# Optimization experiments

Hardware: AMD Instinct MI355X
Metric: run time of the kernel (lower is better)

## Reference

```python
import jax, jax.numpy as jnp
import numpy as np

EPS = 1e-6


def _rmsnorm(x, w, eps=EPS):
    # x: (..., d); normalize over last dim
    ms = jnp.mean(jnp.square(x), axis=-1, keepdims=True)
    return x * jax.lax.rsqrt(ms + eps) * w


def setup_inputs() -> dict:
    key = jax.random.key(0)
    ks = jax.random.split(key, 5)
    B, S, D = 2, 2048, 2048
    n_heads, n_kv = 16, 4
    d_head = D // n_heads  # 128
    sd = 1.0 / np.sqrt(D)
    return {
        "x": jax.random.normal(ks[0], (B, S, D), dtype=jnp.float32),
        "wq": jax.random.normal(ks[1], (D, n_heads * d_head), dtype=jnp.float32) * sd,
        "wk": jax.random.normal(ks[2], (D, n_kv * d_head), dtype=jnp.float32) * sd,
        "wv": jax.random.normal(ks[3], (D, n_kv * d_head), dtype=jnp.float32) * sd,
        "wo": jax.random.normal(ks[4], (D, D), dtype=jnp.float32) * sd,
        "q_norm_w": jnp.ones((d_head,), dtype=jnp.float32),
        "k_norm_w": jnp.ones((d_head,), dtype=jnp.float32),
    }


def reference(x, wq, wk, wv, wo, q_norm_w, k_norm_w):
    B, S, D = x.shape
    n_heads, n_kv = 16, 4
    groups = n_heads // n_kv
    d_head = D // n_heads

    # QKV projections (bias=False)
    q = (x @ wq).reshape(B, S, n_kv, groups, d_head)  # q heads grouped by kv head
    k = (x @ wk).reshape(B, S, n_kv, d_head)
    v = (x @ wv).reshape(B, S, n_kv, d_head)

    # qk RMSNorm over d_head
    q = _rmsnorm(q, q_norm_w)
    k = _rmsnorm(k, k_norm_w)

    # GQA attention without materializing expanded K/V:
    # scores: (B, n_kv, groups, S_q, S_k)
    scale = 1.0 / jnp.sqrt(jnp.asarray(d_head, dtype=x.dtype))
    scores = jnp.einsum('bskgd,btkd->bkgst', q, k) * scale
    causal = jnp.tril(jnp.ones((S, S), dtype=bool))
    scores = jnp.where(causal, scores, jnp.asarray(-jnp.inf, dtype=scores.dtype))
    attn = jax.nn.softmax(scores, axis=-1)
    out = jnp.einsum('bkgst,btkd->bskgd', attn, v)  # (B, S, n_kv, groups, d_head)
    out = out.reshape(B, S, D)
    return out @ wo
```

## Files before the change

### kernel.cpp

```cpp
#include <hip/hip_runtime.h>
#include <hip/hip_bf16.h>
#include <stdint.h>

typedef unsigned short u16;
typedef __attribute__((ext_vector_type(8))) short short8;
typedef __attribute__((ext_vector_type(4))) float f32x4;
typedef __attribute__((ext_vector_type(16))) float f32x16;

__device__ __forceinline__ u16 f2bf(float f){
  union { __hip_bfloat16 h; u16 u; } v; v.h = __float2bfloat16(f); return v.u;
}
__device__ __forceinline__ float bf2f(u16 h){
  union { uint32_t u; float f; } v; v.u = ((uint32_t)h) << 16;
  return v.f;
}
__device__ __forceinline__ f32x4 mfma16(short8 a, short8 b, f32x4 c){
  return __builtin_amdgcn_mfma_f32_16x16x32_bf16(a, b, c, 0, 0, 0);
}
__device__ __forceinline__ f32x16 mfma32(short8 a, short8 b, f32x16 c){
  return __builtin_amdgcn_mfma_f32_32x32x16_bf16(a, b, c, 0, 0, 0);
}
__device__ __forceinline__ void gl_lds16(const u16* g, u16* l){
  __builtin_amdgcn_global_load_lds((const __attribute__((address_space(1))) void*)g,
                                   (__attribute__((address_space(3))) void*)l, 16, 0, 0);
}
template<int N> __device__ __forceinline__ void waitvm(){
  if constexpr (N==0) asm volatile("s_waitcnt vmcnt(0)" ::: "memory");
  else if constexpr (N==4) asm volatile("s_waitcnt vmcnt(4)" ::: "memory");
  else if constexpr (N==8) asm volatile("s_waitcnt vmcnt(8)" ::: "memory");
  else static_assert(N==0 || N==4 || N==8, "unsupported vmcnt");
}
__device__ __forceinline__ void phase_sep(){
  __builtin_amdgcn_sched_barrier(0);
  __builtin_amdgcn_s_barrier();
  __builtin_amdgcn_sched_barrier(0);
}
__device__ __forceinline__ uint32_t cvtpk(float lo, float hi){
  uint32_t r;
  asm("v_cvt_pk_bf16_f32 %0, %1, %2" : "=v"(r) : "v"(lo), "v"(hi));
  return r;
}

__global__ __launch_bounds__(256) void cvt_x(const float* __restrict__ s,
                                             u16* __restrict__ d, int n4){
  const int i = blockIdx.x*256 + threadIdx.x;
  if (i >= n4) return;
  const float4 v = ((const float4*)s)[i];
  ushort4 pk;
  pk.x = f2bf(v.x); pk.y = f2bf(v.y); pk.z = f2bf(v.z); pk.w = f2bf(v.w);
  ((ushort4*)d)[i] = pk;
}

__global__ __launch_bounds__(256) void transpose_cvt(const float* __restrict__ src,
    u16* __restrict__ dst, int R, int C)
{
  __shared__ float tile[32][33];
  const int tx = threadIdx.x, ty = threadIdx.y;
  const int c0 = blockIdx.x << 5, r0 = blockIdx.y << 5;
  #pragma unroll
  for (int i=0;i<4;i++)
    tile[ty + (i<<3)][tx] = src[(size_t)(r0 + ty + (i<<3))*C + c0 + tx];
  __syncthreads();
  #pragma unroll
  for (int i=0;i<4;i++)
    dst[(size_t)(c0 + ty + (i<<3))*R + r0 + tx] = f2bf(tile[tx][ty + (i<<3)]);
}

__global__ __launch_bounds__(256) void v_transpose(const u16* __restrict__ qkv,
    u16* __restrict__ vT)
{
  __shared__ u16 tile[32][33];
  const int tx = threadIdx.x, ty = threadIdx.y;
  const int s0 = blockIdx.x << 5, d0 = blockIdx.y << 5;
  const int bk = blockIdx.z; const int b = bk >> 2, kv = bk & 3;
  const u16* src = qkv + (size_t)b*2048*3072 + 2560 + kv*128;
  #pragma unroll
  for (int i=0;i<4;i++)
    tile[ty + (i<<3)][tx] = src[(size_t)(s0 + ty + (i<<3))*3072 + d0 + tx];
  __syncthreads();
  u16* dst = vT + (size_t)((b<<2)+kv)*128*2048;
  #pragma unroll
  for (int i=0;i<4;i++)
    dst[(size_t)(d0 + ty + (i<<3))*2048 + s0 + tx] = tile[tx][ty + (i<<3)];
}

__global__ __launch_bounds__(256) void rmsnorm_qk(u16* __restrict__ qkv,
    const float* __restrict__ qw, const float* __restrict__ kw)
{
  const int lane = threadIdx.x & 63;
  const int rid = blockIdx.x*4 + (threadIdx.x >> 6);
  const int row = rid / 20;
  const int slot = rid % 20;
  u16* p = qkv + (size_t)row*3072 + slot*128 + (lane<<1);
  const u16 r0 = p[0], r1 = p[1];
  const float a = bf2f(r0), c = bf2f(r1);
  float ss = a*a + c*c;
  #pragma unroll
  for (int off=1; off<64; off<<=1) ss += __shfl_xor(ss, off);
  float sc = rsqrtf(ss*(1.0f/128.0f) + 1e-6f);
  if (slot < 16) sc *= 0.1275187952317199f;
  const float* wp = (slot < 16) ? qw : kw;
  const float w0 = wp[lane<<1], w1 = wp[(lane<<1)+1];
  p[0] = f2bf(a*sc*w0);
  p[1] = f2bf(c*sc*w1);
}

template<int CBF16>
__global__ __launch_bounds__(512, 2) void gemm8(const u16* __restrict__ A,
    const u16* __restrict__ BT, void* __restrict__ Cp,
    int M, int N, int K, int ldc)
{
  __shared__ u16 lds[65536];
  const int tid = threadIdx.x;
  const int w = tid >> 6, lane = tid & 63;
  const int l15 = lane & 15, lg = lane >> 4;
  const int wm = w >> 2, wn = w & 3;
  const int nbx = N >> 8;
  const int nwg = gridDim.x;
  int bid = blockIdx.x;
  bid = (bid & 7) * (nwg >> 3) + (bid >> 3);
  const int m0 = (bid / nbx) << 8;
  const int n0 = (bid % nbx) << 8;

  const u16* gA0 = A  + (size_t)m0*K;
  const u16* gA1 = gA0 + (size_t)128*K;
  const u16* gB0 = BT + (size_t)n0*K;
  const u16* gB1 = gB0 + (size_t)128*K;

  auto slot = [&](int d, int s)->u16*{ return lds + (((d<<2)+s)<<13); };

  auto stage_half = [&](const u16* gbase, int kt, u16* sbase){
    #pragma unroll
    for (int i=0;i<2;i++){
      const int p = (i<<9) + tid;
      const int row = p>>3, sg = (p&7) ^ (row&7);
      gl_lds16(gbase + (size_t)row*K + (kt<<6) + (sg<<3), sbase + (p<<3));
    }
  };
  auto frag_at = [&](const u16* buf, int lrow, int kk)->short8{
    const int s = ((kk<<2)+lg) ^ (lrow&7);
    return *(const short8*)(buf + (((lrow<<3)+s)<<3));
  };

  short8 af[4][2], bfe[2][2], bfo[2][2];
  f32x4 acc[8][4];
  #pragma unroll
  for (int m=0;m<8;m++)
    #pragma unroll
    for (int n=0;n<4;n++) acc[m][n] = (f32x4){0.f,0.f,0.f,0.f};

  const int bh = 2 + (wn>>1);
  const int brow0 = ((wn&1)<<6) + l15;

  auto rd_a = [&](const u16* buf, int mq){
    #pragma unroll
    for (int m=0;m<4;m++)
      #pragma unroll
      for (int kk=0;kk<2;kk++)
        af[m][kk] = frag_at(buf, (mq<<6) + (m<<4) + l15, kk);
  };
  auto rd_b = [&](const u16* buf, int nq, short8 (*dst)[2]){
    #pragma unroll
    for (int n=0;n<2;n++)
      #pragma unroll
      for (int kk=0;kk<2;kk++)
        dst[n][kk] = frag_at(buf, brow0 + (nq<<5) + (n<<4), kk);
  };
  auto do_mfma = [&](int mb, int nb, short8 (*bf)[2]){
    __builtin_amdgcn_s_setprio(1);
    #pragma unroll
    for (int m=0;m<4;m++)
      #pragma unroll
      for (int n=0;n<2;n++)
        #pragma unroll
        for (int kk=0;kk<2;kk++)
          acc[mb+m][nb+n] = mfma16(af[m][kk], bf[n][kk], acc[mb+m][nb+n]);
    __builtin_amdgcn_s_setprio(0);
  };

  stage_half(gA0, 0, slot(0,0)); stage_half(gA1, 0, slot(0,1));
  stage_half(gB0, 0, slot(0,2)); stage_half(gB1, 0, slot(0,3));
  stage_half(gA0, 1, slot(1,0)); stage_half(gA1, 1, slot(1,1));
  waitvm<4>();
  phase_sep();

  const int niter = K >> 7;
  for (int i=0; i<niter; ++i){
    const bool full = (i+1 < niter);
    const int t1 = 2*i+1;
    rd_a(slot(0,wm), 0); rd_b(slot(0,bh), 0, bfe);
    stage_half(gB0, t1, slot(1,2)); stage_half(gB1, t1, slot(1,3));
    phase_sep();
    do_mfma(0, 0, bfe);
    phase_sep();
    rd_b(slot(0,bh), 1, bfo);
    phase_sep();
    do_mfma(0, 2, bfo);
    phase_sep();
    rd_a(slot(0,wm), 1);
    phase_sep();
    do_mfma(4, 2, bfo);
    phase_sep();
    rd_b(slot(0,bh), 0, bfe);
    if (full){ stage_half(gA0, t1+1, slot(0,0)); stage_half(gA1, t1+1, slot(0,1)); }
    phase_sep();
    do_mfma(4, 0, bfe);
    if (full) waitvm<4>(); else waitvm<0>();
    phase_sep();
    rd_a(slot(1,wm), 0); rd_b(slot(1,bh), 0, bfe);
    if (full){ stage_half(gB0, t1+1, slot(0,2)); stage_half(gB1, t1+1, slot(0,3)); }
    phase_sep();
    do_mfma(0, 0, bfe);
    phase_sep();
    rd_b(slot(1,bh), 1, bfo);
    phase_sep();
    do_mfma(0, 2, bfo);
    phase_sep();
    rd_a(slot(1,wm), 1);
    phase_sep();
    do_mfma(4, 2, bfo);
    phase_sep();
    rd_b(slot(1,bh), 0, bfe);
    if (full){ stage_half(gA0, t1+2, slot(1,0)); stage_half(gA1, t1+2, slot(1,1)); }
    phase_sep();
    do_mfma(4, 0, bfe);
    if (full) waitvm<4>();
    phase_sep();
  }

  #pragma unroll
  for (int m=0;m<8;m++){
    #pragma unroll
    for (int n=0;n<4;n++){
      const int col = n0 + (wn<<6) + (n<<4) + l15;
      #pragma unroll
      for (int r=0;r<4;r++){
        const int row = m0 + (wm<<7) + (m<<4) + (lg<<2) + r;
        if (CBF16) ((u16*)Cp)[(size_t)row*ldc + col] = f2bf(acc[m][n][r]);
        else       ((float*)Cp)[(size_t)row*ldc + col] = acc[m][n][r];
      }
    }
  }
}

__global__ __launch_bounds__(256, 2) void attn_kernel(const u16* __restrict__ qkv,
    const u16* __restrict__ vT, u16* __restrict__ aout)
{
  __shared__ u16 Klds[2][8192];
  __shared__ u16 Vlds[8192];
  const int tid = threadIdx.x;
  const int w = tid >> 6, lane = tid & 63;
  const int l31 = lane & 31, hi = lane >> 5;
  const int bx = blockIdx.x, h = blockIdx.y, b = blockIdx.z;
  const int qI = b ? bx : (15 - bx);
  const int kvh = h >> 2;
  const int qb = qI*128 + (w<<5);
  const int nt = 2*qI + 2;

  const u16* qkvb = qkv + (size_t)b*2048*3072;
  short8 qf[8];
  {
    const u16* qp = qkvb + (size_t)(qb + l31)*3072 + h*128 + hi*8;
    #pragma unroll
    for (int kk=0;kk<8;kk++) qf[kk] = *(const short8*)(qp + kk*16);
  }
  f32x16 oacc[4];
  #pragma unroll
  for (int d=0;d<4;d++)
    #pragma unroll
    for (int r=0;r<16;r++) oacc[d][r] = 0.f;
  float m_run = -__builtin_inff(), lsum = 0.f;

  const u16* kb_ = qkvb + 2048 + kvh*128;
  const u16* vb_ = vT + (size_t)((b<<2)+kvh)*128*2048;

  auto stageK = [&](int t, int buf){
    #pragma unroll
    for (int i=0;i<4;i++){
      const int u = (i<<8) + tid;
      const int row = u>>4, d0 = (u&15) ^ (row&15);
      gl_lds16(kb_ + (size_t)((t<<6)+row)*3072 + (d0<<3), &Klds[buf][u<<3]);
    }
  };
  auto stageV = [&](int t){
    #pragma unroll
    for (int i=0;i<4;i++){
      const int u = (i<<8) + tid;
      const int rp = u>>4, z = (u&15) ^ (rp&15);
      const int d = (rp<<1) + (z>>3), k8 = z&7;
      gl_lds16(vb_ + (size_t)d*2048 + (t<<6) + (k8<<3), &Vlds[u<<3]);
    }
  };

  stageK(0, 0);
  int kbuf = 0;
  for (int t=0; t<nt; ++t){
    const bool pre = (t+1 < nt);
    stageV(t);
    if (pre) stageK(t+1, kbuf^1);
    if (pre) waitvm<8>(); else waitvm<4>();
    phase_sep();
    const int t0 = t<<6;
    const bool act = (t0 <= qb + 31);
    uint32_t paw[4][4];
    if (act){
      f32x16 s0, s1;
      #pragma unroll
      for (int r=0;r<16;r++){ s0[r] = 0.f; s1[r] = 0.f; }
      #pragma unroll
      for (int kk=0;kk<8;kk++){
        const int d0 = (kk<<1) + hi;
        const short8 k0 = *(const short8*)&Klds[kbuf][((l31<<4) + (d0 ^ (l31&15)))<<3];
        s0 = mfma32(k0, qf[kk], s0);
        const int r1 = 32 + l31;
        const short8 k1 = *(const short8*)&Klds[kbuf][((r1<<4) + (d0 ^ (r1&15)))<<3];
        s1 = mfma32(k1, qf[kk], s1);
      }
      if (t0 + 63 > qb){
        const int qrel = qb + l31 - t0;
        #pragma unroll
        for (int r=0;r<16;r++){
          const int kloc = (r&3) + ((r>>2)<<3) + (hi<<2);
          if (kloc      > qrel) s0[r] = -__builtin_inff();
          if (kloc + 32 > qrel) s1[r] = -__builtin_inff();
        }
      }
      float t8[8];
      #pragma unroll
      for (int i=0;i<8;i++) t8[i] = fmaxf(fmaxf(s0[i], s0[i+8]), fmaxf(s1[i], s1[i+8]));
      #pragma unroll
      for (int i=0;i<4;i++) t8[i] = fmaxf(t8[i], t8[i+4]);
      float mx = fmaxf(fmaxf(t8[0],t8[1]), fmaxf(t8[2],t8[3]));
      mx = fmaxf(mx, __shfl_xor(mx, 32));
      const bool noskip = !__all(mx - m_run <= 8.0f);
      const float mnew = noskip ? fmaxf(m_run, mx) : m_run;
      float rs = 0.f;
      #pragma unroll
      for (int i=0;i<16;i++){
        s0[i] = __builtin_amdgcn_exp2f(s0[i] - mnew);
        s1[i] = __builtin_amdgcn_exp2f(s1[i] - mnew);
        rs += s0[i] + s1[i];
      }
      rs += __shfl_xor(rs, 32);
      if (noskip){
        const float corr = __builtin_amdgcn_exp2f(m_run - mnew);
        m_run = mnew;
        lsum = lsum*corr + rs;
        #pragma unroll
        for (int r=0;r<16;r++){
          const float cr = __shfl(corr, (r&3) + ((r>>2)<<3) + (hi<<2));
          #pragma unroll
          for (int db=0;db<4;db++) oacc[db][r] *= cr;
        }
      } else {
        lsum += rs;
      }
      #pragma unroll
      for (int kk=0;kk<4;kk++){
        const int base = (kk&1)<<3;
        float v0,v1,v2,v3,v4,v5,v6,v7;
        if (kk<2){ v0=s0[base+0]; v1=s0[base+1]; v2=s0[base+2]; v3=s0[base+3];
                   v4=s0[base+4]; v5=s0[base+5]; v6=s0[base+6]; v7=s0[base+7]; }
        else     { v0=s1[base+0]; v1=s1[base+1]; v2=s1[base+2]; v3=s1[base+3];
                   v4=s1[base+4]; v5=s1[base+5]; v6=s1[base+6]; v7=s1[base+7]; }
        uint32_t a0 = cvtpk(v0, v1), a1 = cvtpk(v2, v3);
        uint32_t b0 = cvtpk(v4, v5), b1 = cvtpk(v6, v7);
        asm volatile("v_permlane32_swap_b32 %0, %1" : "+v"(a0), "+v"(b0));
        asm volatile("v_permlane32_swap_b32 %0, %1" : "+v"(a1), "+v"(b1));
        paw[kk][0] = a0; paw[kk][1] = a1; paw[kk][2] = b0; paw[kk][3] = b1;
      }
    }
    if (pre) waitvm<4>(); else waitvm<0>();
    phase_sep();
    if (act){
      #pragma unroll
      for (int kk=0;kk<4;kk++){
        union { uint32_t w[4]; short8 v; } pu;
        pu.w[0]=paw[kk][0]; pu.w[1]=paw[kk][1]; pu.w[2]=paw[kk][2]; pu.w[3]=paw[kk][3];
        const short8 pa = pu.v;
        #pragma unroll
        for (int db=0;db<4;db++){
          const int d = (db<<5) + l31, rp = d>>1;
          const int sl = (((d&1)<<3) | ((kk<<1)+hi)) ^ (rp&15);
          const short8 vv = *(const short8*)&Vlds[((rp<<4)+sl)<<3];
          oacc[db] = mfma32(pa, vv, oacc[db]);
        }
      }
    }
    phase_sep();
    kbuf ^= 1;
  }

  const float inv = 1.0f / lsum;
  #pragma unroll
  for (int r=0;r<16;r++){
    const int qr = (r&3) + ((r>>2)<<3) + (hi<<2);
    const float ivr = __shfl(inv, qr);
    u16* op = aout + (size_t)(b*2048 + qb + qr)*2048 + h*128 + l31;
    #pragma unroll
    for (int db=0;db<4;db++)
      op[db<<5] = f2bf(oacc[db][r] * ivr);
  }
}

extern "C" void kernel_launch(void* const* d_in, const int* in_sizes, int n_in,
                              void* d_out, int out_size, void* d_ws, size_t ws_size,
                              hipStream_t stream) {
  const float* x  = (const float*)d_in[0];
  const float* wq = (const float*)d_in[1];
  const float* wk = (const float*)d_in[2];
  const float* wv = (const float*)d_in[3];
  const float* wo = (const float*)d_in[4];
  const float* qw = (const float*)d_in[5];
  const float* kw = (const float*)d_in[6];
  char* ws = (char*)d_ws;
  u16* xbf   = (u16*)(ws);
  u16* wqkvT = (u16*)(ws + 16777216);
  u16* woT   = (u16*)(ws + 29360128);
  u16* qkv   = (u16*)(ws + 37748736);
  u16* vT    = (u16*)(ws + 62914560);
  float* out = (float*)d_out;

  dim3 tb(32,8);
  cvt_x<<<8192, 256, 0, stream>>>(x, xbf, 2097152);
  transpose_cvt<<<dim3(64,64), tb, 0, stream>>>(wq, wqkvT,             2048, 2048);
  transpose_cvt<<<dim3(16,64), tb, 0, stream>>>(wk, wqkvT + 2048*2048, 2048, 512);
  transpose_cvt<<<dim3(16,64), tb, 0, stream>>>(wv, wqkvT + 2560*2048, 2048, 512);
  transpose_cvt<<<dim3(64,64), tb, 0, stream>>>(wo, woT,               2048, 2048);
  gemm8<1><<<192, 512, 0, stream>>>(xbf, wqkvT, qkv, 4096, 3072, 2048, 3072);
  rmsnorm_qk<<<20480, 256, 0, stream>>>(qkv, qw, kw);
  v_transpose<<<dim3(64,4,8), tb, 0, stream>>>(qkv, vT);
  attn_kernel<<<dim3(16,16,2), 256, 0, stream>>>(qkv, vT, xbf);
  gemm8<0><<<128, 512, 0, stream>>>(xbf, woT, out, 4096, 2048, 2048, 2048);
}
```

Before: 214.0 us.

## Pair high and low query tiles per block and double-buffer K/V staging

Each wave now handles 16 query rows from a high tile and 16 from a mirrored low tile, so every block runs the same number of key tiles (32 - p) and causal work stays balanced. The per-tile activity skip is removed, and masking now runs on every tile. V gets its own double buffer alongside K, and tiles are prefetched two steps ahead with a single wait per iteration, which removes the mid-iteration V wait. The cost is double the LDS for V, which may lower occupancy, plus masking and exp work on tiles where the low rows are fully masked.

New measurement: 229.8 us. +7.4%, slower.

```diff
diff --git a/kernel.cpp b/kernel.cpp
--- a/kernel.cpp
+++ b/kernel.cpp
@@ -247,20 +247,21 @@
     const u16* __restrict__ vT, u16* __restrict__ aout)
 {
   __shared__ u16 Klds[2][8192];
-  __shared__ u16 Vlds[8192];
+  __shared__ u16 Vlds[2][8192];
   const int tid = threadIdx.x;
   const int w = tid >> 6, lane = tid & 63;
   const int l31 = lane & 31, hi = lane >> 5;
   const int bx = blockIdx.x, h = blockIdx.y, b = blockIdx.z;
-  const int qI = b ? bx : (15 - bx);
+  const int p_eff = b ? (15 - bx) : bx;
   const int kvh = h >> 2;
-  const int qb = qI*128 + (w<<5);
-  const int nt = 2*qI + 2;
+  const int hq0 = (31 - p_eff) << 6, lq0 = p_eff << 6;
+  const int nt = 32 - p_eff;
+  const int qrow = (l31 < 16) ? (hq0 + (w<<4) + l31) : (lq0 + (w<<4) + l31 - 16);
 
   const u16* qkvb = qkv + (size_t)b*2048*3072;
   short8 qf[8];
   {
-    const u16* qp = qkvb + (size_t)(qb + l31)*3072 + h*128 + hi*8;
+    const u16* qp = qkvb + (size_t)qrow*3072 + h*128 + hi*8;
     #pragma unroll
     for (int kk=0;kk<8;kk++) qf[kk] = *(const short8*)(qp + kk*16);
   }
@@ -274,129 +275,119 @@
   const u16* kb_ = qkvb + 2048 + kvh*128;
   const u16* vb_ = vT + (size_t)((b<<2)+kvh)*128*2048;
 
-  auto stageK = [&](int t, int buf){
+  auto stageKV = [&](int t, int buf){
     #pragma unroll
     for (int i=0;i<4;i++){
       const int u = (i<<8) + tid;
       const int row = u>>4, d0 = (u&15) ^ (row&15);
       gl_lds16(kb_ + (size_t)((t<<6)+row)*3072 + (d0<<3), &Klds[buf][u<<3]);
     }
-  };
-  auto stageV = [&](int t){
     #pragma unroll
     for (int i=0;i<4;i++){
       const int u = (i<<8) + tid;
       const int rp = u>>4, z = (u&15) ^ (rp&15);
       const int d = (rp<<1) + (z>>3), k8 = z&7;
-      gl_lds16(vb_ + (size_t)d*2048 + (t<<6) + (k8<<3), &Vlds[u<<3]);
-    }
-  };
-
-  stageK(0, 0);
-  int kbuf = 0;
+      gl_lds16(vb_ + (size_t)d*2048 + (t<<6) + (k8<<3), &Vlds[buf][u<<3]);
+    }
+  };
+
+  stageKV(0, 0);
+  if (nt > 1) stageKV(1, 1);
   for (int t=0; t<nt; ++t){
-    const bool pre = (t+1 < nt);
-    stageV(t);
-    if (pre) stageK(t+1, kbuf^1);
-    if (pre) waitvm<8>(); else waitvm<4>();
+    const int kbuf = t & 1;
+    if (t+1 < nt) waitvm<8>(); else waitvm<0>();
     phase_sep();
     const int t0 = t<<6;
-    const bool act = (t0 <= qb + 31);
+    f32x16 s0, s1;
+    #pragma unroll
+    for (int r=0;r<16;r++){ s0[r] = 0.f; s1[r] = 0.f; }
+    #pragma unroll
+    for (int kk=0;kk<8;kk++){
+      const int d0 = (kk<<1) + hi;
+      const short8 k0 = *(const short8*)&Klds[kbuf][((l31<<4) + (d0 ^ (l31&15)))<<3];
+      s0 = mfma32(k0, qf[kk], s0);
+      const int r1 = 32 + l31;
+      const short8 k1 = *(const short8*)&Klds[kbuf][((r1<<4) + (d0 ^ (r1&15)))<<3];
+      s1 = mfma32(k1, qf[kk], s1);
+    }
+    {
+      const int qrel = qrow - t0;
+      #pragma unroll
+      for (int r=0;r<16;r++){
+        const int kloc = (r&3) + ((r>>2)<<3) + (hi<<2);
+        if (kloc      > qrel) s0[r] = -__builtin_inff();
+        if (kloc + 32 > qrel) s1[r] = -__builtin_inff();
+      }
+    }
+    float t8[8];
+    #pragma unroll
+    for (int i=0;i<8;i++) t8[i] = fmaxf(fmaxf(s0[i], s0[i+8]), fmaxf(s1[i], s1[i+8]));
+    #pragma unroll
+    for (int i=0;i<4;i++) t8[i] = fmaxf(t8[i], t8[i+4]);
+    float mx = fmaxf(fmaxf(t8[0],t8[1]), fmaxf(t8[2],t8[3]));
+    mx = fmaxf(mx, __shfl_xor(mx, 32));
+    const bool noskip = !__all(mx - m_run <= 8.0f);
+    const float mnew = noskip ? fmaxf(m_run, mx) : m_run;
+    float rs = 0.f;
+    #pragma unroll
+    for (int i=0;i<16;i++){
+      s0[i] = __builtin_amdgcn_exp2f(s0[i] - mnew);
+      s1[i] = __builtin_amdgcn_exp2f(s1[i] - mnew);
+      rs += s0[i] + s1[i];
+    }
+    rs += __shfl_xor(rs, 32);
+    if (noskip){
+      const float corr = __builtin_amdgcn_exp2f(m_run - mnew);
+      m_run = mnew;
+      lsum = lsum*corr + rs;
+      #pragma unroll
+      for (int r=0;r<16;r++){
+        const float cr = __shfl(corr, (r&3) + ((r>>2)<<3) + (hi<<2));
+        #pragma unroll
+        for (int db=0;db<4;db++) oacc[db][r] *= cr;
+      }
+    } else {
+      lsum += rs;
+    }
     uint32_t paw[4][4];
-    if (act){
-      f32x16 s0, s1;
-      #pragma unroll
-      for (int r=0;r<16;r++){ s0[r] = 0.f; s1[r] = 0.f; }
-      #pragma unroll
-      for (int kk=0;kk<8;kk++){
-        const int d0 = (kk<<1) + hi;
-        const short8 k0 = *(const short8*)&Klds[kbuf][((l31<<4) + (d0 ^ (l31&15)))<<3];
-        s0 = mfma32(k0, qf[kk], s0);
-        const int r1 = 32 + l31;
-        const short8 k1 = *(const short8*)&Klds[kbuf][((r1<<4) + (d0 ^ (r1&15)))<<3];
-        s1 = mfma32(k1, qf[kk], s1);
+    #pragma unroll
+    for (int kk=0;kk<4;kk++){
+      const int base = (kk&1)<<3;
+      float v0,v1,v2,v3,v4,v5,v6,v7;
+      if (kk<2){ v0=s0[base+0]; v1=s0[base+1]; v2=s0[base+2]; v3=s0[base+3];
+                 v4=s0[base+4]; v5=s0[base+5]; v6=s0[base+6]; v7=s0[base+7]; }
+      else     { v0=s1[base+0]; v1=s1[base+1]; v2=s1[base+2]; v3=s1[base+3];
+                 v4=s1[base+4]; v5=s1[base+5]; v6=s1[base+6]; v7=s1[base+7]; }
+      uint32_t a0 = cvtpk(v0, v1), a1 = cvtpk(v2, v3);
+      uint32_t b0 = cvtpk(v4, v5), b1 = cvtpk(v6, v7);
+      asm volatile("v_permlane32_swap_b32 %0, %1" : "+v"(a0), "+v"(b0));
+      asm volatile("v_permlane32_swap_b32 %0, %1" : "+v"(a1), "+v"(b1));
+      paw[kk][0] = a0; paw[kk][1] = a1; paw[kk][2] = b0; paw[kk][3] = b1;
+    }
+    #pragma unroll
+    for (int kk=0;kk<4;kk++){
+      union { uint32_t w[4]; short8 v; } pu;
+      pu.w[0]=paw[kk][0]; pu.w[1]=paw[kk][1]; pu.w[2]=paw[kk][2]; pu.w[3]=paw[kk][3];
+      const short8 pa = pu.v;
+      #pragma unroll
+      for (int db=0;db<4;db++){
+        const int d = (db<<5) + l31, rp = d>>1;
+        const int sl = (((d&1)<<3) | ((kk<<1)+hi)) ^ (rp&15);
+        const short8 vv = *(const short8*)&Vlds[kbuf][((rp<<4)+sl)<<3];
+        oacc[db] = mfma32(pa, vv, oacc[db]);
       }
-      if (t0 + 63 > qb){
-        const int qrel = qb + l31 - t0;
-        #pragma unroll
-        for (int r=0;r<16;r++){
-          const int kloc = (r&3) + ((r>>2)<<3) + (hi<<2);
-          if (kloc      > qrel) s0[r] = -__builtin_inff();
-          if (kloc + 32 > qrel) s1[r] = -__builtin_inff();
-        }
-      }
-      float t8[8];
-      #pragma unroll
-      for (int i=0;i<8;i++) t8[i] = fmaxf(fmaxf(s0[i], s0[i+8]), fmaxf(s1[i], s1[i+8]));
-      #pragma unroll
-      for (int i=0;i<4;i++) t8[i] = fmaxf(t8[i], t8[i+4]);
-      float mx = fmaxf(fmaxf(t8[0],t8[1]), fmaxf(t8[2],t8[3]));
-      mx = fmaxf(mx, __shfl_xor(mx, 32));
-      const bool noskip = !__all(mx - m_run <= 8.0f);
-      const float mnew = noskip ? fmaxf(m_run, mx) : m_run;
-      float rs = 0.f;
-      #pragma unroll
-      for (int i=0;i<16;i++){
-        s0[i] = __builtin_amdgcn_exp2f(s0[i] - mnew);
-        s1[i] = __builtin_amdgcn_exp2f(s1[i] - mnew);
-        rs += s0[i] + s1[i];
-      }
-      rs += __shfl_xor(rs, 32);
-      if (noskip){
-        const float corr = __builtin_amdgcn_exp2f(m_run - mnew);
-        m_run = mnew;
-        lsum = lsum*corr + rs;
-        #pragma unroll
-        for (int r=0;r<16;r++){
-          const float cr = __shfl(corr, (r&3) + ((r>>2)<<3) + (hi<<2));
-          #pragma unroll
-          for (int db=0;db<4;db++) oacc[db][r] *= cr;
-        }
-      } else {
-        lsum += rs;
-      }
-      #pragma unroll
-      for (int kk=0;kk<4;kk++){
-        const int base = (kk&1)<<3;
-        float v0,v1,v2,v3,v4,v5,v6,v7;
-        if (kk<2){ v0=s0[base+0]; v1=s0[base+1]; v2=s0[base+2]; v3=s0[base+3];
-                   v4=s0[base+4]; v5=s0[base+5]; v6=s0[base+6]; v7=s0[base+7]; }
-        else     { v0=s1[base+0]; v1=s1[base+1]; v2=s1[base+2]; v3=s1[base+3];
-                   v4=s1[base+4]; v5=s1[base+5]; v6=s1[base+6]; v7=s1[base+7]; }
-        uint32_t a0 = cvtpk(v0, v1), a1 = cvtpk(v2, v3);
-        uint32_t b0 = cvtpk(v4, v5), b1 = cvtpk(v6, v7);
-        asm volatile("v_permlane32_swap_b32 %0, %1" : "+v"(a0), "+v"(b0));
-        asm volatile("v_permlane32_swap_b32 %0, %1" : "+v"(a1), "+v"(b1));
-        paw[kk][0] = a0; paw[kk][1] = a1; paw[kk][2] = b0; paw[kk][3] = b1;
-      }
-    }
-    if (pre) waitvm<4>(); else waitvm<0>();
-    phase_sep();
-    if (act){
-      #pragma unroll
-      for (int kk=0;kk<4;kk++){
-        union { uint32_t w[4]; short8 v; } pu;
-        pu.w[0]=paw[kk][0]; pu.w[1]=paw[kk][1]; pu.w[2]=paw[kk][2]; pu.w[3]=paw[kk][3];
-        const short8 pa = pu.v;
-        #pragma unroll
-        for (int db=0;db<4;db++){
-          const int d = (db<<5) + l31, rp = d>>1;
-          const int sl = (((d&1)<<3) | ((kk<<1)+hi)) ^ (rp&15);
-          const short8 vv = *(const short8*)&Vlds[((rp<<4)+sl)<<3];
-          oacc[db] = mfma32(pa, vv, oacc[db]);
-        }
-      }
-    }
-    phase_sep();
-    kbuf ^= 1;
+    }
+    phase_sep();
+    if (t+2 < nt) stageKV(t+2, kbuf);
   }
 
   const float inv = 1.0f / lsum;
   #pragma unroll
   for (int r=0;r<16;r++){
-    const int qr = (r&3) + ((r>>2)<<3) + (hi<<2);
-    const float ivr = __shfl(inv, qr);
-    u16* op = aout + (size_t)(b*2048 + qb + qr)*2048 + h*128 + l31;
+    const int qp_ = (r&3) + ((r>>2)<<3) + (hi<<2);
+    const float ivr = __shfl(inv, qp_);
+    const int grow = (qp_ < 16) ? (hq0 + (w<<4) + qp_) : (lq0 + (w<<4) + qp_ - 16);
+    u16* op = aout + (size_t)(b*2048 + grow)*2048 + h*128 + l31;
     #pragma unroll
     for (int db=0;db<4;db++)
       op[db<<5] = f2bf(oacc[db][r] * ivr);
```
